# Kernel tuning notes

Measured on AMD Instinct MI355X. Metric: run time of the kernel, lower is better.

Reference implementation:

```python
import jax, jax.numpy as jnp
import numpy as np

B, T, V, E = 8, 256, 32000, 512
ENC_H, DEC_H, DEC_IN = 512, 512, 512
MAX_OOVS = 100


def setup_inputs() -> dict:
    key = jax.random.key(0)
    ks = jax.random.split(key, 7)
    output_logits = jax.random.normal(ks[0], (B, T, V), dtype=jnp.float32)
    attn_weights = jax.random.uniform(ks[1], (B, T, E), dtype=jnp.float32)
    decoder_hidden_state = jax.random.normal(ks[2], (B, T, 2 * DEC_H), dtype=jnp.float32)
    decoder_input = jax.random.normal(ks[3], (B, T, DEC_IN), dtype=jnp.float32)
    context_vector = jax.random.normal(ks[4], (B, T, ENC_H), dtype=jnp.float32)
    encoder_input = jax.random.randint(ks[5], (B, E), 0, V + MAX_OOVS, dtype=jnp.int64)
    pgen_w = jax.random.normal(ks[6], (1, ENC_H + 2 * DEC_H + DEC_IN), dtype=jnp.float32) * 0.02
    pgen_b = jnp.zeros((1,), dtype=jnp.float32)
    return {
        "output_logits": output_logits,
        "attn_weights": attn_weights,
        "decoder_hidden_state": decoder_hidden_state,
        "decoder_input": decoder_input,
        "context_vector": context_vector,
        "encoder_input": encoder_input,
        "pgen_w": pgen_w,
        "pgen_b": pgen_b,
        "max_oovs": MAX_OOVS,
    }


def reference(output_logits, attn_weights, decoder_hidden_state, decoder_input,
              context_vector, encoder_input, pgen_w, pgen_b, max_oovs):
    b, t, v = output_logits.shape
    # softmax over vocab, then zero-pad to extended vocab [b, t, v + max_oovs]
    probs = jax.nn.softmax(output_logits, axis=-1)
    probs_ext = jnp.pad(probs, ((0, 0), (0, 0), (0, max_oovs)))
    # pgen = sigmoid(Linear([context; dec_hidden; dec_input]))  -> [b, t, 1]
    pre = jnp.concatenate([context_vector, decoder_hidden_state, decoder_input], axis=-1)
    pgen = jax.nn.sigmoid(jnp.einsum('btf,of->bto', pre, pgen_w) + pgen_b)
    pcopy = 1.0 - pgen
    # scatter_add attention weights into extended-vocab copy distribution
    bi = jnp.arange(b)[:, None, None]           # [b,1,1]
    ti = jnp.arange(t)[None, :, None]           # [1,t,1]
    idx = encoder_input[:, None, :]             # [b,1,E] broadcast over t
    copy_probs = jnp.zeros_like(probs_ext).at[bi, ti, idx].add(attn_weights)
    total = pgen * probs_ext + pcopy * copy_probs
    return (total, pgen)
```

## Files before the change

### kernel.cpp

```cpp
#include <hip/hip_runtime.h>
#include <cmath>

#define B_    8
#define T_    256
#define V_    32000
#define E_    512
#define OOV_  100
#define VE_   (V_ + OOV_)
#define ROWS_ (B_ * T_)
#define NV4_  (V_ / 4)
#define PAD4_ (OOV_ / 4)
#define TOTAL_ ((size_t)ROWS_ * VE_)

__global__ __launch_bounds__(1024) void pg_softmax_kernel(
    const float* __restrict__ logits,
    const float* __restrict__ ctx,
    const float* __restrict__ hid,
    const float* __restrict__ dec,
    const float* __restrict__ pw,
    const float* __restrict__ pb,
    float* __restrict__ out_total,
    float* __restrict__ out_pgen)
{
  const int row  = blockIdx.x;
  const int tid  = threadIdx.x;
  const int lane = tid & 63;
  const int wid  = tid >> 6;
  __shared__ float redA[16];
  __shared__ float redB[16];

  float acc = 0.f;
  #pragma unroll
  for (int k = 0; k < 2; ++k) {
    const int f = tid + (k << 10);
    float pv;
    if (f < 512)       pv = ctx[row * 512 + f];
    else if (f < 1536) pv = hid[row * 1024 + (f - 512)];
    else               pv = dec[row * 512 + (f - 1536)];
    acc += pv * pw[f];
  }
  #pragma unroll
  for (int o = 32; o > 0; o >>= 1) acc += __shfl_xor(acc, o);
  if (lane == 0) redA[wid] = acc;
  __syncthreads();
  if (tid < 16) {
    float x = redA[tid];
    #pragma unroll
    for (int o = 8; o > 0; o >>= 1) x += __shfl_xor(x, o);
    if (tid == 0) redA[0] = x;
  }
  __syncthreads();
  const float pgen = 1.f / (1.f + __expf(-(redA[0] + pb[0])));
  __syncthreads();

  const float4* lrow = (const float4*)(logits + (size_t)row * V_);
  float4 v[8];
  float m = -3.0e38f;
  #pragma unroll
  for (int k = 0; k < 8; ++k) {
    const int i = tid + (k << 10);
    if (i < NV4_) {
      const float4 x = lrow[i];
      v[k] = x;
      m = fmaxf(m, fmaxf(fmaxf(x.x, x.y), fmaxf(x.z, x.w)));
    }
  }
  float s = 0.f;
  #pragma unroll
  for (int k = 0; k < 8; ++k) {
    const int i = tid + (k << 10);
    if (i < NV4_) {
      float4 x = v[k];
      x.x = __expf(x.x - m); x.y = __expf(x.y - m);
      x.z = __expf(x.z - m); x.w = __expf(x.w - m);
      s += x.x + x.y + x.z + x.w;
      v[k] = x;
    }
  }
  #pragma unroll
  for (int o = 32; o > 0; o >>= 1) {
    const float om = __shfl_xor(m, o);
    const float os = __shfl_xor(s, o);
    const float nm = fmaxf(m, om);
    s = s * __expf(m - nm) + os * __expf(om - nm);
    m = nm;
  }
  if (lane == 0) { redA[wid] = m; redB[wid] = s; }
  __syncthreads();
  if (tid < 16) {
    float mm = redA[tid], ss = redB[tid];
    #pragma unroll
    for (int o = 8; o > 0; o >>= 1) {
      const float om = __shfl_xor(mm, o);
      const float os = __shfl_xor(ss, o);
      const float nm = fmaxf(mm, om);
      ss = ss * __expf(mm - nm) + os * __expf(om - nm);
      mm = nm;
    }
    if (tid == 0) { redA[0] = mm; redB[0] = ss; }
  }
  __syncthreads();
  const float M = redA[0];
  const float S = redB[0];
  const float scale = pgen * __expf(m - M) / S;

  float4* orow = (float4*)(out_total + (size_t)row * VE_);
  #pragma unroll
  for (int k = 0; k < 8; ++k) {
    const int i = tid + (k << 10);
    if (i < NV4_) {
      float4 x = v[k];
      x.x *= scale; x.y *= scale; x.z *= scale; x.w *= scale;
      orow[i] = x;
    }
  }
  if (tid < PAD4_) orow[NV4_ + tid] = make_float4(0.f, 0.f, 0.f, 0.f);
  if (tid == 0) out_pgen[row] = pgen;
}

__global__ __launch_bounds__(256) void scatter_kernel(
    const float* __restrict__ attn,
    const int*   __restrict__ enc,
    const float* __restrict__ pgen,
    float* __restrict__ out_total)
{
  const int g  = blockIdx.x * 256 + threadIdx.x;
  const int e  = g & (E_ - 1);
  const int bt = g >> 9;
  const int b  = bt >> 8;
  const int idx = enc[(b << 9) + e];
  const float add = (1.f - pgen[bt]) * attn[g];
  atomicAdd(out_total + (size_t)bt * VE_ + idx, add);
}

extern "C" void kernel_launch(void* const* d_in, const int* in_sizes, int n_in,
                              void* d_out, int out_size, void* d_ws, size_t ws_size,
                              hipStream_t stream) {
  const float* logits = (const float*)d_in[0];
  const float* attn   = (const float*)d_in[1];
  const float* hid    = (const float*)d_in[2];
  const float* dec    = (const float*)d_in[3];
  const float* ctx    = (const float*)d_in[4];
  const int*   enc    = (const int*)d_in[5];
  const float* pw     = (const float*)d_in[6];
  const float* pb     = (const float*)d_in[7];

  float* out_total = (float*)d_out;
  float* out_pgen  = out_total + TOTAL_;

  pg_softmax_kernel<<<ROWS_, 1024, 0, stream>>>(
      logits, ctx, hid, dec, pw, pb, out_total, out_pgen);
  scatter_kernel<<<(ROWS_ * E_) / 256, 256, 0, stream>>>(
      attn, enc, out_pgen, out_total);
}
```

Measured before the change: 510.9 us.

## Fuse copy-distribution scatter into softmax kernel and specialize tail loop

Merges the separate scatter kernel into the softmax/pgen kernel: each row block loads its attention weights and encoder indices up front, then after writing the scaled softmax row it does block-local unsafe atomic adds of (1-pgen)*attn into the same row. This removes one kernel launch and the second kernel's re-read of pgen and of output lines. The vocab loop is also specialized so only the last float4 chunk is bounds-checked. A __syncthreads orders the plain stores before the atomics; unsafeAtomicAdd may use hardware float atomics that behave differently on fine-grained memory.

```diff
diff --git a/kernel.cpp b/kernel.cpp
--- a/kernel.cpp
+++ b/kernel.cpp
@@ -12,11 +12,13 @@
 #define PAD4_ (OOV_ / 4)
 #define TOTAL_ ((size_t)ROWS_ * VE_)
 
-__global__ __launch_bounds__(1024) void pg_softmax_kernel(
+__global__ __launch_bounds__(1024) void pg_fused_kernel(
     const float* __restrict__ logits,
+    const float* __restrict__ attn,
     const float* __restrict__ ctx,
     const float* __restrict__ hid,
     const float* __restrict__ dec,
+    const int*   __restrict__ enc,
     const float* __restrict__ pw,
     const float* __restrict__ pb,
     float* __restrict__ out_total,
@@ -28,6 +30,13 @@
   const int wid  = tid >> 6;
   __shared__ float redA[16];
   __shared__ float redB[16];
+
+  float att_v = 0.f;
+  int   att_i = 0;
+  if (tid < E_) {
+    att_v = attn[row * E_ + tid];
+    att_i = enc[((row >> 8) << 9) + tid];
+  }
 
   float acc = 0.f;
   #pragma unroll
@@ -57,19 +66,20 @@
   float4 v[8];
   float m = -3.0e38f;
   #pragma unroll
-  for (int k = 0; k < 8; ++k) {
-    const int i = tid + (k << 10);
-    if (i < NV4_) {
-      const float4 x = lrow[i];
-      v[k] = x;
-      m = fmaxf(m, fmaxf(fmaxf(x.x, x.y), fmaxf(x.z, x.w)));
-    }
+  for (int k = 0; k < 7; ++k) {
+    const float4 x = lrow[tid + (k << 10)];
+    v[k] = x;
+    m = fmaxf(m, fmaxf(fmaxf(x.x, x.y), fmaxf(x.z, x.w)));
+  }
+  if (tid < NV4_ - 7168) {
+    const float4 x = lrow[tid + 7168];
+    v[7] = x;
+    m = fmaxf(m, fmaxf(fmaxf(x.x, x.y), fmaxf(x.z, x.w)));
   }
   float s = 0.f;
   #pragma unroll
   for (int k = 0; k < 8; ++k) {
-    const int i = tid + (k << 10);
-    if (i < NV4_) {
+    if (k < 7 || tid < NV4_ - 7168) {
       float4 x = v[k];
       x.x = __expf(x.x - m); x.y = __expf(x.y - m);
       x.z = __expf(x.z - m); x.w = __expf(x.w - m);
@@ -107,30 +117,20 @@
   float4* orow = (float4*)(out_total + (size_t)row * VE_);
   #pragma unroll
   for (int k = 0; k < 8; ++k) {
-    const int i = tid + (k << 10);
-    if (i < NV4_) {
+    if (k < 7 || tid < NV4_ - 7168) {
       float4 x = v[k];
       x.x *= scale; x.y *= scale; x.z *= scale; x.w *= scale;
-      orow[i] = x;
+      orow[tid + (k << 10)] = x;
     }
   }
   if (tid < PAD4_) orow[NV4_ + tid] = make_float4(0.f, 0.f, 0.f, 0.f);
   if (tid == 0) out_pgen[row] = pgen;
-}
 
-__global__ __launch_bounds__(256) void scatter_kernel(
-    const float* __restrict__ attn,
-    const int*   __restrict__ enc,
-    const float* __restrict__ pgen,
-    float* __restrict__ out_total)
-{
-  const int g  = blockIdx.x * 256 + threadIdx.x;
-  const int e  = g & (E_ - 1);
-  const int bt = g >> 9;
-  const int b  = bt >> 8;
-  const int idx = enc[(b << 9) + e];
-  const float add = (1.f - pgen[bt]) * attn[g];
-  atomicAdd(out_total + (size_t)bt * VE_ + idx, add);
+  __syncthreads();
+  if (tid < E_) {
+    unsafeAtomicAdd(out_total + (size_t)row * VE_ + att_i,
+                    (1.f - pgen) * att_v);
+  }
 }
 
 extern "C" void kernel_launch(void* const* d_in, const int* in_sizes, int n_in,
@@ -148,8 +148,6 @@
   float* out_total = (float*)d_out;
   float* out_pgen  = out_total + TOTAL_;
 
-  pg_softmax_kernel<<<ROWS_, 1024, 0, stream>>>(
-      logits, ctx, hid, dec, pw, pb, out_total, out_pgen);
-  scatter_kernel<<<(ROWS_ * E_) / 256, 256, 0, stream>>>(
-      attn, enc, out_pgen, out_total);
+  pg_fused_kernel<<<ROWS_, 1024, 0, stream>>>(
+      logits, attn, ctx, hid, dec, enc, pw, pb, out_total, out_pgen);
 }
```

Result: no change. 512.4 us (+0.3%).
